# Kernel tuning notes

Measured on AMD Instinct MI355X. Metric: run time of the kernel, lower is better.

The kernel has to match this reference:

```python
import jax, jax.numpy as jnp
import numpy as np

B, S, D, H = 1, 4096, 1024, 16
HD = D // H  # head_dim = 64
NEG = -1e9


def _rotate_half(x):
    x1, x2 = jnp.split(x, 2, axis=-1)
    return jnp.concatenate([-x2, x1], axis=-1)


def _apply_rope(x, cos, sin):
    # x: [b, s, h, hd]; cos/sin: [s, hd] -> broadcast over batch and heads
    c = cos[None, :, None, :]
    s = sin[None, :, None, :]
    return x * c + _rotate_half(x) * s


def setup_inputs() -> dict:
    key = jax.random.key(0)
    kx, kq, ko = jax.random.split(key, 3)
    x = jax.random.normal(kx, (B, S, D), dtype=jnp.float32)
    # causal additive mask (finite large-negative for safe grads)
    i = jnp.arange(S)
    attn_mask = jnp.where(i[None, :] > i[:, None], NEG, 0.0).astype(jnp.float32)[None, None]
    # standard RoPE tables
    inv_freq = 1.0 / (10000.0 ** (np.arange(0, HD, 2, dtype=np.float32) / HD))
    ang = np.arange(S, dtype=np.float32)[:, None] * inv_freq[None, :]  # [S, HD/2]
    ang = np.concatenate([ang, ang], axis=-1)  # [S, HD]
    rope_cos = jnp.asarray(np.cos(ang))
    rope_sin = jnp.asarray(np.sin(ang))
    W_qkv = jax.random.normal(kq, (D, 3 * D), dtype=jnp.float32) * (D ** -0.5)
    W_out = jax.random.normal(ko, (D, D), dtype=jnp.float32) * (D ** -0.5)
    return {"x": x, "attn_mask": attn_mask, "rope_cos": rope_cos,
            "rope_sin": rope_sin, "W_qkv": W_qkv, "W_out": W_out}


def reference(x, attn_mask, rope_cos, rope_sin, W_qkv, W_out):
    b, s, d = x.shape
    qkv = x @ W_qkv                              # [b, s, 3d]
    q, k, v = jnp.split(qkv, 3, axis=-1)
    q = q.reshape(b, s, H, HD)
    k = k.reshape(b, s, H, HD)
    v = v.reshape(b, s, H, HD)
    q = _apply_rope(q, rope_cos, rope_sin)
    k = _apply_rope(k, rope_cos, rope_sin)
    att = jnp.einsum('bqhd,bkhd->bhqk', q, k) / jnp.sqrt(jnp.float32(HD))
    att = att + attn_mask                        # additive mask broadcast [b,h,s,s]
    att = jax.nn.softmax(att, axis=-1)
    out = jnp.einsum('bhqk,bkhd->bqhd', att, v).reshape(b, s, d)
    return out @ W_out
```

## Files before the change

### kernel.cpp

```cpp
#include <hip/hip_runtime.h>


typedef __attribute__((ext_vector_type(8)))  __bf16 bf16x8;
typedef __attribute__((ext_vector_type(4)))  float  f32x4;
typedef __attribute__((ext_vector_type(16))) float  f32x16;
typedef __attribute__((ext_vector_type(8)))  unsigned short ushort8;
typedef __attribute__((ext_vector_type(4)))  unsigned int   u32x4;

#define MFMA16(a,b,c) __builtin_amdgcn_mfma_f32_16x16x32_bf16((a),(b),(c),0,0,0)
#define MFMA32(a,b,c) __builtin_amdgcn_mfma_f32_32x32x16_bf16((a),(b),(c),0,0,0)

static __device__ __forceinline__ unsigned short f2bf(float f) {
  unsigned int u = __builtin_bit_cast(unsigned int, f);
  u = (u + 0x7FFFu + ((u >> 16) & 1u)) >> 16;
  return (unsigned short)u;
}
static __device__ __forceinline__ float bf2f(unsigned short u) {
  return __builtin_bit_cast(float, (unsigned int)u << 16);
}
static __device__ __forceinline__ unsigned int cvtpk(float a, float b) {
  unsigned int r;
  asm("v_cvt_pk_bf16_f32 %0, %1, %2" : "=v"(r) : "v"(a), "v"(b));
  return r;
}
static __device__ __forceinline__ void plswap(unsigned int& a, unsigned int& b) {
#if __has_builtin(__builtin_amdgcn_permlane32_swap)
  auto r = __builtin_amdgcn_permlane32_swap(a, b, false, false);
  a = r[0]; b = r[1];
#else
  unsigned int xa = (unsigned int)__shfl_xor((int)a, 32);
  unsigned int xb = (unsigned int)__shfl_xor((int)b, 32);
  int lane = __builtin_amdgcn_mbcnt_hi(~0u, __builtin_amdgcn_mbcnt_lo(~0u, 0));
  bool hi = lane >= 32;
  a = hi ? xb : a;
  b = hi ? b : xa;
#endif
}
static __device__ __forceinline__ void gll16(const unsigned short* gp, const unsigned short* lp) {
  unsigned int m0v = __builtin_amdgcn_readfirstlane((unsigned int)(unsigned long long)(uintptr_t)lp);
  asm volatile("s_mov_b32 m0, %0\n\tglobal_load_lds_dwordx4 %1, off"
               :: "s"(m0v), "v"(gp) : "memory");
}
static __device__ __forceinline__ void wait_dma() {
  asm volatile("s_waitcnt vmcnt(0)" ::: "memory");
}

__global__ void convert_x(const float* __restrict__ x, unsigned short* __restrict__ o) {
  int i = (blockIdx.x * 256 + threadIdx.x) * 4;
  float4 v = *reinterpret_cast<const float4*>(x + i);
  ushort4 u;
  u.x = f2bf(v.x); u.y = f2bf(v.y); u.z = f2bf(v.z); u.w = f2bf(v.w);
  *reinterpret_cast<ushort4*>(o + i) = u;
}

__global__ void transpose_w(const float* __restrict__ W, unsigned short* __restrict__ WT,
                            int R, int C) {
  __shared__ float t[32][33];
  int c0 = blockIdx.x * 32, r0 = blockIdx.y * 32;
  int tx = threadIdx.x, ty = threadIdx.y;
#pragma unroll
  for (int i = 0; i < 32; i += 8)
    t[ty + i][tx] = W[(size_t)(r0 + ty + i) * C + c0 + tx];
  __syncthreads();
#pragma unroll
  for (int i = 0; i < 32; i += 8)
    WT[(size_t)(c0 + ty + i) * R + r0 + tx] = f2bf(t[tx][ty + i]);
}

template <typename OutT>
__global__ __launch_bounds__(256) void gemm_lds(const unsigned short* __restrict__ A,
                                                const unsigned short* __restrict__ BT,
                                                OutT* __restrict__ C, int M, int N, int K) {
  __shared__ __align__(16) unsigned short As[128 * 32];
  __shared__ __align__(16) unsigned short Bs[128 * 32];
  int tid = threadIdx.x;
  int lane = tid & 63, w = tid >> 6;
  int wr = w >> 1, wc = w & 1;
  int row0 = blockIdx.y * 128, col0 = blockIdx.x * 128;
  int lr = lane & 15, lk = lane >> 4;
  f32x4 acc[4][4] = {};
  for (int k0 = 0; k0 < K; k0 += 32) {
#pragma unroll
    for (int i = 0; i < 2; ++i) {
      int c = i * 256 + tid;
      int r = c >> 2, cc = (c & 3) * 8;
      gll16(A  + (size_t)(row0 + r) * K + k0 + cc, &As[i * 2048 + w * 512]);
      gll16(BT + (size_t)(col0 + r) * K + k0 + cc, &Bs[i * 2048 + w * 512]);
    }
    wait_dma();
    __syncthreads();
    bf16x8 a[4], b[4];
#pragma unroll
    for (int m = 0; m < 4; m++)
      a[m] = *reinterpret_cast<const bf16x8*>(&As[(wr * 64 + m * 16 + lr) * 32 + lk * 8]);
#pragma unroll
    for (int n = 0; n < 4; n++)
      b[n] = *reinterpret_cast<const bf16x8*>(&Bs[(wc * 64 + n * 16 + lr) * 32 + lk * 8]);
#pragma unroll
    for (int m = 0; m < 4; m++)
#pragma unroll
      for (int n = 0; n < 4; n++)
        acc[m][n] = MFMA16(a[m], b[n], acc[m][n]);
    __syncthreads();
  }
#pragma unroll
  for (int m = 0; m < 4; m++)
#pragma unroll
    for (int n = 0; n < 4; n++)
#pragma unroll
      for (int r = 0; r < 4; r++) {
        size_t off = (size_t)(row0 + wr * 64 + m * 16 + lk * 4 + r) * N + col0 + wc * 64 + n * 16 + lr;
        if constexpr (sizeof(OutT) == 2) C[off] = f2bf(acc[m][n][r]);
        else                             C[off] = acc[m][n][r];
      }
}

__global__ void rope_qk(const unsigned short* __restrict__ qkv,
                        const float* __restrict__ cosb, const float* __restrict__ sinb,
                        unsigned short* __restrict__ Q, unsigned short* __restrict__ K) {
  const float QSCALE = 0.125f * 1.4426950408889634f;
  int idx = blockIdx.x * 256 + threadIdx.x;
  int c = idx & 7, s = (idx >> 3) & 4095, h = idx >> 15;
  int d0 = c * 8;
  int base = s * 3072 + h * 64;
  ushort8 qv  = *reinterpret_cast<const ushort8*>(qkv + base + d0);
  ushort8 qv2 = *reinterpret_cast<const ushort8*>(qkv + base + (d0 ^ 32));
  ushort8 kv  = *reinterpret_cast<const ushort8*>(qkv + base + 1024 + d0);
  ushort8 kv2 = *reinterpret_cast<const ushort8*>(qkv + base + 1024 + (d0 ^ 32));
  float sign = (d0 < 32) ? -1.f : 1.f;
  const float4* cp = reinterpret_cast<const float4*>(cosb + s * 64 + d0);
  const float4* sp = reinterpret_cast<const float4*>(sinb + s * 64 + d0);
  float4 c0 = cp[0], c1 = cp[1], s0 = sp[0], s1 = sp[1];
  float co[8] = {c0.x, c0.y, c0.z, c0.w, c1.x, c1.y, c1.z, c1.w};
  float si[8] = {s0.x, s0.y, s0.z, s0.w, s1.x, s1.y, s1.z, s1.w};
  ushort8 qo, ko;
#pragma unroll
  for (int j = 0; j < 8; ++j) {
    float q = bf2f(qv[j]), q2 = bf2f(qv2[j]);
    float k = bf2f(kv[j]), k2 = bf2f(kv2[j]);
    qo[j] = f2bf((q * co[j] + sign * q2 * si[j]) * QSCALE);
    ko[j] = f2bf(k * co[j] + sign * k2 * si[j]);
  }
  *reinterpret_cast<ushort8*>(Q + (size_t)h * 262144 + (size_t)s * 64 + d0) = qo;
  int tt = s >> 5, ql = s & 31, lo = (d0 >> 3) & 1, f = d0 >> 4;
  size_t koff = (size_t)h * 262144 + (size_t)tt * 2048 + (size_t)f * 512
              + (size_t)(lo * 32 + ql) * 8;
  *reinterpret_cast<ushort8*>(K + koff) = ko;
}

__global__ __launch_bounds__(256) void v_frag_prep(const unsigned short* __restrict__ qkv,
                                                   unsigned short* __restrict__ VF) {
  __shared__ unsigned short tile[32][68];
  int t = blockIdx.x, h = blockIdx.y;
  int tid = threadIdx.x;
  {
    int r = tid >> 3, c8 = (tid & 7) * 8;
    *reinterpret_cast<ushort8*>(&tile[r][c8]) =
        *reinterpret_cast<const ushort8*>(qkv + (size_t)(t * 32 + r) * 3072 + 2048 + h * 64 + c8);
  }
  __syncthreads();
  int f = tid >> 6, lane = tid & 63;
  int ql = lane & 31, lo = lane >> 5;
  int sb = (f & 1) * 16 + lo * 8;
  int d  = (f >> 1) * 32 + ql;
  ushort8 v;
#pragma unroll
  for (int j = 0; j < 8; ++j) v[j] = tile[sb + j][d];
  *reinterpret_cast<ushort8*>(VF + (size_t)h * 262144 + (size_t)t * 2048
                              + (size_t)f * 512 + (size_t)lane * 8) = v;
}

__global__ __launch_bounds__(256) void flash_attn32(const unsigned short* __restrict__ Q,
                                                    const unsigned short* __restrict__ Kf,
                                                    const unsigned short* __restrict__ Vf,
                                                    unsigned short* __restrict__ O) {
  const int S = 4096;
  const float FM = 16.0f;
  __shared__ float mrg[3][64][34];
  int flat = blockIdx.x;
  int virt = (flat & 7) * 128 + (flat >> 3);
  int h  = virt >> 6;
  int pr = virt & 63;
  int tid = threadIdx.x;
  int lane = tid & 63, w = tid >> 6;
  int ql = lane & 31, lo = lane >> 5;
  const unsigned short* Qh = Q  + (size_t)h * S * 64;
  const unsigned short* Kh = Kf + (size_t)h * S * 64 + lane * 8;
  const unsigned short* Vh = Vf + (size_t)h * S * 64 + lane * 8;

  auto run_tile = [&](int qt) {
    int q0 = qt * 32;
    const int nt = qt + 1;
    bf16x8 qf[4];
#pragma unroll
    for (int f = 0; f < 4; ++f)
      qf[f] = *reinterpret_cast<const bf16x8*>(Qh + (q0 + ql) * 64 + f * 16 + lo * 8);
    f32x16 oT0 = {}, oT1 = {};
    float l = 0.f;

    bf16x8 kA[4], kB[4];
    auto loadK = [&](bf16x8* kf, int tt) {
#pragma unroll
      for (int f = 0; f < 4; ++f)
        kf[f] = *reinterpret_cast<const bf16x8*>(Kh + (size_t)tt * 2048 + f * 512);
    };
    auto QK = [&](bf16x8* kf) {
      f32x16 p = {};
      __builtin_amdgcn_s_setprio(1);
#pragma unroll
      for (int f = 0; f < 4; ++f) p = MFMA32(kf[f], qf[f], p);
      __builtin_amdgcn_s_setprio(0);
      return p;
    };
    auto SOFTPV = [&](f32x16& p, int tcur) {
      const unsigned short* vp = Vh + (size_t)tcur * 2048;
      bf16x8 v00 = *reinterpret_cast<const bf16x8*>(vp);
      bf16x8 v01 = *reinterpret_cast<const bf16x8*>(vp + 512);
      bf16x8 v10 = *reinterpret_cast<const bf16x8*>(vp + 1024);
      bf16x8 v11 = *reinterpret_cast<const bf16x8*>(vp + 1536);
      if (tcur == nt - 1) {
#pragma unroll
        for (int r = 0; r < 16; ++r) {
          int kvr = (r & 3) + 8 * (r >> 2) + 4 * lo;
          if (kvr > ql) p[r] = -1e9f;
        }
      }
#pragma unroll
      for (int r = 0; r < 16; ++r) { p[r] = __builtin_amdgcn_exp2f(p[r] - FM); l += p[r]; }
      unsigned int A0 = cvtpk(p[0],  p[1]),  A1 = cvtpk(p[2],  p[3]);
      unsigned int B0 = cvtpk(p[4],  p[5]),  B1 = cvtpk(p[6],  p[7]);
      plswap(A0, B0); plswap(A1, B1);
      u32x4 w0 = {A0, A1, B0, B1};
      bf16x8 P0 = __builtin_bit_cast(bf16x8, w0);
      unsigned int C0 = cvtpk(p[8],  p[9]),  C1 = cvtpk(p[10], p[11]);
      unsigned int D0 = cvtpk(p[12], p[13]), D1 = cvtpk(p[14], p[15]);
      plswap(C0, D0); plswap(C1, D1);
      u32x4 w1 = {C0, C1, D0, D1};
      bf16x8 P1 = __builtin_bit_cast(bf16x8, w1);
      __builtin_amdgcn_s_setprio(1);
      oT0 = MFMA32(v00, P0, oT0);
      oT0 = MFMA32(v01, P1, oT0);
      oT1 = MFMA32(v10, P0, oT1);
      oT1 = MFMA32(v11, P1, oT1);
      __builtin_amdgcn_s_setprio(0);
    };

    int t = w;
    if (t < nt) {
      loadK(kA, t);
      f32x16 pA = QK(kA);
      f32x16 pB;
      if (t + 4 < nt) loadK(kB, t + 4);
      while (true) {
        if (t + 4 < nt) pB = QK(kB);
        if (t + 8 < nt) loadK(kA, t + 8);
        SOFTPV(pA, t);
        t += 4; if (t >= nt) break;
        if (t + 4 < nt) pA = QK(kA);
        if (t + 8 < nt) loadK(kB, t + 8);
        SOFTPV(pB, t);
        t += 4; if (t >= nt) break;
      }
    }

    if (w > 0) {
#pragma unroll
      for (int r = 0; r < 16; ++r) {
        mrg[w - 1][lane][r]      = oT0[r];
        mrg[w - 1][lane][16 + r] = oT1[r];
      }
      mrg[w - 1][lane][32] = l;
    }
    __syncthreads();
    if (w == 0) {
#pragma unroll
      for (int j = 0; j < 3; ++j) {
#pragma unroll
        for (int r = 0; r < 16; ++r) {
          oT0[r] += mrg[j][lane][r];
          oT1[r] += mrg[j][lane][16 + r];
        }
        l += mrg[j][lane][32];
      }
      l += __shfl_xor(l, 32);
      float rl = 1.0f / l;
      size_t obase = (size_t)(q0 + ql) * 1024 + h * 64;
#pragma unroll
      for (int r = 0; r < 16; ++r) {
        int d = (r & 3) + 8 * (r >> 2) + 4 * lo;
        O[obase + d]      = f2bf(oT0[r] * rl);
        O[obase + 32 + d] = f2bf(oT1[r] * rl);
      }
    }
    __syncthreads();
  };

  run_tile(127 - pr);
  run_tile(pr);
}

extern "C" void kernel_launch(void* const* d_in, const int* in_sizes, int n_in,
                              void* d_out, int out_size, void* d_ws, size_t ws_size,
                              hipStream_t stream) {
  const float* x        = (const float*)d_in[0];
  const float* rope_cos = (const float*)d_in[2];
  const float* rope_sin = (const float*)d_in[3];
  const float* W_qkv    = (const float*)d_in[4];
  const float* W_out    = (const float*)d_in[5];
  float* out = (float*)d_out;

  char* ws = (char*)d_ws;
  const size_t MB = 1u << 20;
  unsigned short* xbf   = (unsigned short*)(ws + 0 * MB);
  unsigned short* WqkvT = (unsigned short*)(ws + 8 * MB);
  unsigned short* WoutT = (unsigned short*)(ws + 14 * MB);
  unsigned short* qkv   = (unsigned short*)(ws + 16 * MB);
  unsigned short* Qb    = (unsigned short*)(ws + 40 * MB);
  unsigned short* Kfb   = (unsigned short*)(ws + 48 * MB);
  unsigned short* Vfb   = (unsigned short*)(ws + 56 * MB);
  unsigned short* Ob    = (unsigned short*)(ws + 64 * MB);

  convert_x<<<4096, 256, 0, stream>>>(x, xbf);
  transpose_w<<<dim3(3072 / 32, 1024 / 32), dim3(32, 8), 0, stream>>>(W_qkv, WqkvT, 1024, 3072);
  transpose_w<<<dim3(1024 / 32, 1024 / 32), dim3(32, 8), 0, stream>>>(W_out, WoutT, 1024, 1024);

  gemm_lds<unsigned short><<<dim3(3072 / 128, 4096 / 128), 256, 0, stream>>>(
      xbf, WqkvT, qkv, 4096, 3072, 1024);

  rope_qk<<<2048, 256, 0, stream>>>(qkv, rope_cos, rope_sin, Qb, Kfb);
  v_frag_prep<<<dim3(128, 16), 256, 0, stream>>>(qkv, Vfb);

  flash_attn32<<<1024, 256, 0, stream>>>(Qb, Kfb, Vfb, Ob);

  gemm_lds<float><<<dim3(1024 / 128, 4096 / 128), 256, 0, stream>>>(
      Ob, WoutT, out, 4096, 1024, 1024);
}
```

Before: 153.9 us.

## Prefetch V before QK, interleave PV MFMAs, tree-reduce row sum, set occupancy

After: 253.6 us. 1.65x slower.

```diff
diff --git a/kernel.cpp b/kernel.cpp
--- a/kernel.cpp
+++ b/kernel.cpp
@@ -170,10 +170,10 @@
                               + (size_t)f * 512 + (size_t)lane * 8) = v;
 }
 
-__global__ __launch_bounds__(256) void flash_attn32(const unsigned short* __restrict__ Q,
-                                                    const unsigned short* __restrict__ Kf,
-                                                    const unsigned short* __restrict__ Vf,
-                                                    unsigned short* __restrict__ O) {
+__global__ __launch_bounds__(256, 4) void flash_attn32(const unsigned short* __restrict__ Q,
+                                                       const unsigned short* __restrict__ Kf,
+                                                       const unsigned short* __restrict__ Vf,
+                                                       unsigned short* __restrict__ O) {
   const int S = 4096;
   const float FM = 16.0f;
   __shared__ float mrg[3][64][34];
@@ -198,11 +198,16 @@
     f32x16 oT0 = {}, oT1 = {};
     float l = 0.f;
 
-    bf16x8 kA[4], kB[4];
+    bf16x8 kA[4], kB[4], vC[4];
     auto loadK = [&](bf16x8* kf, int tt) {
 #pragma unroll
       for (int f = 0; f < 4; ++f)
         kf[f] = *reinterpret_cast<const bf16x8*>(Kh + (size_t)tt * 2048 + f * 512);
+    };
+    auto loadV = [&](int tt) {
+#pragma unroll
+      for (int f = 0; f < 4; ++f)
+        vC[f] = *reinterpret_cast<const bf16x8*>(Vh + (size_t)tt * 2048 + f * 512);
     };
     auto QK = [&](bf16x8* kf) {
       f32x16 p = {};
@@ -213,11 +218,6 @@
       return p;
     };
     auto SOFTPV = [&](f32x16& p, int tcur) {
-      const unsigned short* vp = Vh + (size_t)tcur * 2048;
-      bf16x8 v00 = *reinterpret_cast<const bf16x8*>(vp);
-      bf16x8 v01 = *reinterpret_cast<const bf16x8*>(vp + 512);
-      bf16x8 v10 = *reinterpret_cast<const bf16x8*>(vp + 1024);
-      bf16x8 v11 = *reinterpret_cast<const bf16x8*>(vp + 1536);
       if (tcur == nt - 1) {
 #pragma unroll
         for (int r = 0; r < 16; ++r) {
@@ -226,7 +226,14 @@
         }
       }
 #pragma unroll
-      for (int r = 0; r < 16; ++r) { p[r] = __builtin_amdgcn_exp2f(p[r] - FM); l += p[r]; }
+      for (int r = 0; r < 16; ++r) p[r] = __builtin_amdgcn_exp2f(p[r] - FM);
+      {
+        float s0 = (p[0] + p[1])   + (p[2] + p[3]);
+        float s1 = (p[4] + p[5])   + (p[6] + p[7]);
+        float s2 = (p[8] + p[9])   + (p[10] + p[11]);
+        float s3 = (p[12] + p[13]) + (p[14] + p[15]);
+        l += (s0 + s1) + (s2 + s3);
+      }
       unsigned int A0 = cvtpk(p[0],  p[1]),  A1 = cvtpk(p[2],  p[3]);
       unsigned int B0 = cvtpk(p[4],  p[5]),  B1 = cvtpk(p[6],  p[7]);
       plswap(A0, B0); plswap(A1, B1);
@@ -238,10 +245,10 @@
       u32x4 w1 = {C0, C1, D0, D1};
       bf16x8 P1 = __builtin_bit_cast(bf16x8, w1);
       __builtin_amdgcn_s_setprio(1);
-      oT0 = MFMA32(v00, P0, oT0);
-      oT0 = MFMA32(v01, P1, oT0);
-      oT1 = MFMA32(v10, P0, oT1);
-      oT1 = MFMA32(v11, P1, oT1);
+      oT0 = MFMA32(vC[0], P0, oT0);
+      oT1 = MFMA32(vC[2], P0, oT1);
+      oT0 = MFMA32(vC[1], P1, oT0);
+      oT1 = MFMA32(vC[3], P1, oT1);
       __builtin_amdgcn_s_setprio(0);
     };
 
@@ -252,10 +259,12 @@
       f32x16 pB;
       if (t + 4 < nt) loadK(kB, t + 4);
       while (true) {
+        loadV(t);
         if (t + 4 < nt) pB = QK(kB);
         if (t + 8 < nt) loadK(kA, t + 8);
         SOFTPV(pA, t);
         t += 4; if (t >= nt) break;
+        loadV(t);
         if (t + 4 < nt) pA = QK(kA);
         if (t + 8 < nt) loadK(kB, t + 8);
         SOFTPV(pB, t);
```
